# Kernel optimization log

Measured on AMD Instinct MI355X. Metric: run time of the kernel, lower is better.

Reference implementation:

```python
import jax, jax.numpy as jnp
import numpy as np


def _hippo_scale_params(N, L):
    """Replicates HiPPOScale.__init__ for discretization='bilinear' (pure numpy)."""
    q = np.arange(N, dtype=np.float64)
    col, row = np.meshgrid(q, q)
    r = 2 * q + 1
    M = -(np.where(row >= col, r, 0) - np.diag(q))
    T = np.sqrt(np.diag(2 * q + 1))
    A = T @ M @ np.linalg.inv(T)          # (N, N)
    B = np.diag(T)                         # (N,)
    ts = np.arange(1, L + 1, dtype=np.float64)[:, None, None]  # (L,1,1)
    At = A[None] / ts                      # A / t, batched over t
    I = np.eye(N, dtype=np.float64)
    Mm = I[None] - 0.5 * At
    Nn = I[None] + 0.5 * At
    A_stacked = np.linalg.solve(Mm, Nn)                      # (L, N, N)
    Bt = B[None, :] / ts[:, 0, :]                             # (L, N)
    B_stacked = np.linalg.solve(Mm, Bt[..., None])[..., 0]    # (L, N)
    return A_stacked.astype(np.float32), B_stacked.astype(np.float32)


def setup_inputs() -> dict:
    N, L, Bsz = 64, 4096, 64
    key = jax.random.key(0)
    A_st, B_st = _hippo_scale_params(N, L)
    inputs = jax.random.normal(key, (L, Bsz), dtype=jnp.float32)
    return {
        "inputs": inputs,                       # (L, B)
        "A_stacked": jnp.asarray(A_st),         # (L, N, N)
        "B_stacked": jnp.asarray(B_st),         # (L, N)
    }


def reference(inputs, A_stacked, B_stacked):
    # u[t, b, :] = inputs[t, b] * B_stacked[t, :]   -> (L, B, N)
    u = inputs[..., None] * B_stacked[:, None, :]

    # x[t] = A[t] @ x[t-1] + u[t], x[-1] = 0  (time-varying linear recurrence).
    # The torch code computes this via a divide-and-conquer unroll; here we use
    # the equivalent parallel associative scan with elements (A, u) and
    # composition (A2@A1, A2@u1 + u2).
    def combine(e1, e2):
        a1, u1 = e1
        a2, u2 = e2
        a = jnp.matmul(a2, a1)                                  # (l, N, N)
        v = jnp.einsum('...ij,...bj->...bi', a2, u1) + u2       # (l, B, N)
        return (a, v)

    _, x = jax.lax.associative_scan(combine, (A_stacked, u))
    return x  # (L, B, N)
```

## Files before the change

### kernel.cpp

```cpp
#include <hip/hip_runtime.h>

#define TL 4096
#define NB 64
#define CH 8
#define CN 512
#define AS 72

typedef __attribute__((ext_vector_type(8))) short short8;
typedef __attribute__((ext_vector_type(4))) short short4v;
typedef __attribute__((ext_vector_type(4))) float floatx4;

__device__ inline floatx4 mfma_bf16(short8 a, short8 b, floatx4 c) {
    return __builtin_amdgcn_mfma_f32_16x16x32_bf16(a, b, c, 0, 0, 0);
}

__device__ inline void split_bf16(float x, short& h, short& l) {
    union { float f; unsigned u; } v; v.f = x;
    unsigned uh = v.u + 0x7FFFu + ((v.u >> 16) & 1u);
    h = (short)(uh >> 16);
    union { unsigned u; float f; } hv; hv.u = ((unsigned)(unsigned short)h) << 16;
    float r = x - hv.f;
    union { float f; unsigned u; } rv; rv.f = r;
    unsigned ul = rv.u + 0x7FFFu + ((rv.u >> 16) & 1u);
    l = (short)(ul >> 16);
}

__global__ __launch_bounds__(256, 2)
void hippo_phase1(const float* __restrict__ inp, const float* __restrict__ Ag,
                  const float* __restrict__ Bst,
                  float* __restrict__ PT, float* __restrict__ VT)
{
    __shared__ short Ah[NB][AS], Al[NB][AS];
    __shared__ short SBh[NB][AS], SBl[NB][AS];
    __shared__ short VBh[NB][AS], VBl[NB][AS];
    __shared__ float btl[NB], itl[NB];

    const int tid  = threadIdx.x;
    const int c    = blockIdx.x;
    const int t0   = c * CH;
    const int w    = tid >> 6, lane = tid & 63;
    const int quad = lane >> 4, l15 = lane & 15;

#pragma unroll
    for (int q = 0; q < 16; ++q) {
        int f = tid + q * 256;
        int n = f >> 6, k = f & 63;
        SBh[n][k] = (n == k) ? (short)0x3F80 : (short)0;
        SBl[n][k] = 0; VBh[n][k] = 0; VBl[n][k] = 0;
    }

    float4 pre[4];
    {
        const float4* Ap = (const float4*)(Ag + (size_t)t0 * 4096);
#pragma unroll
        for (int q = 0; q < 4; ++q) pre[q] = Ap[tid + q * 256];
    }

    floatx4 accS[4], accV[4];

    for (int s = 0; s < CH; ++s) {
        int t = t0 + s;
#pragma unroll
        for (int q = 0; q < 4; ++q) {
            int f = tid + q * 256;
            int m = f >> 4, k0 = (f & 15) * 4;
            float vv[4] = {pre[q].x, pre[q].y, pre[q].z, pre[q].w};
            short4v h4, l4;
#pragma unroll
            for (int r = 0; r < 4; ++r) { short hh, ll; split_bf16(vv[r], hh, ll); h4[r]=hh; l4[r]=ll; }
            *(short4v*)&Ah[m][k0] = h4;
            *(short4v*)&Al[m][k0] = l4;
        }
        if (tid < 64) { btl[tid] = Bst[(size_t)t*64 + tid]; itl[tid] = inp[(size_t)t*64 + tid]; }
        if (s + 1 < CH) {
            const float4* Ap = (const float4*)(Ag + (size_t)(t+1) * 4096);
#pragma unroll
            for (int q = 0; q < 4; ++q) pre[q] = Ap[tid + q * 256];
        }
        __syncthreads();

#pragma unroll
        for (int ni = 0; ni < 4; ++ni) {
            float ib = itl[16*ni + l15];
#pragma unroll
            for (int r = 0; r < 4; ++r) {
                accS[ni][r] = 0.0f;
                accV[ni][r] = btl[16*w + 4*quad + r] * ib;
            }
        }
#pragma unroll
        for (int kc = 0; kc < 2; ++kc) {
            int ko = 32*kc + 8*quad;
            short8 aH = *(const short8*)&Ah[16*w + l15][ko];
            short8 aL = *(const short8*)&Al[16*w + l15][ko];
#pragma unroll
            for (int ni = 0; ni < 4; ++ni) {
                int n = 16*ni + l15;
                short8 sH = *(const short8*)&SBh[n][ko];
                short8 sL = *(const short8*)&SBl[n][ko];
                accS[ni] = mfma_bf16(aH, sH, accS[ni]);
                accS[ni] = mfma_bf16(aH, sL, accS[ni]);
                accS[ni] = mfma_bf16(aL, sH, accS[ni]);
                short8 vH = *(const short8*)&VBh[n][ko];
                short8 vL = *(const short8*)&VBl[n][ko];
                accV[ni] = mfma_bf16(aH, vH, accV[ni]);
                accV[ni] = mfma_bf16(aH, vL, accV[ni]);
                accV[ni] = mfma_bf16(aL, vH, accV[ni]);
            }
        }
        __syncthreads();

        if (s + 1 < CH) {
#pragma unroll
            for (int ni = 0; ni < 4; ++ni) {
                int cc = 16*ni + l15, r0 = 16*w + 4*quad;
                short4v h4, l4;
#pragma unroll
                for (int r = 0; r < 4; ++r) { short hh,ll; split_bf16(accS[ni][r],hh,ll); h4[r]=hh; l4[r]=ll; }
                *(short4v*)&SBh[cc][r0] = h4; *(short4v*)&SBl[cc][r0] = l4;
#pragma unroll
                for (int r = 0; r < 4; ++r) { short hh,ll; split_bf16(accV[ni][r],hh,ll); h4[r]=hh; l4[r]=ll; }
                *(short4v*)&VBh[cc][r0] = h4; *(short4v*)&VBl[cc][r0] = l4;
            }
        }
    }
#pragma unroll
    for (int ni = 0; ni < 4; ++ni) {
        int cc = 16*ni + l15, r0 = 16*w + 4*quad;
        *(floatx4*)(PT + (size_t)c*4096 + cc*64 + r0) = accS[ni];
        *(floatx4*)(VT + (size_t)c*4096 + cc*64 + r0) = accV[ni];
    }
}

__global__ __launch_bounds__(256, 2)
void hippo_seqscan(float* __restrict__ PT, float* __restrict__ VT,
                   int bstride, int off0, int estride)
{
    __shared__ short PAh[NB][AS], PAl[NB][AS];
    __shared__ short PBh[NB][AS], PBl[NB][AS];
    __shared__ short VBh[NB][AS], VBl[NB][AS];

    const int tid  = threadIdx.x;
    const int base = blockIdx.x * bstride + off0;
    const int w    = tid >> 6, lane = tid & 63;
    const int quad = lane >> 4, l15 = lane & 15;

    {
        const float* p0 = PT + (size_t)base * 4096;
        const float* v0 = VT + (size_t)base * 4096;
#pragma unroll
        for (int q = 0; q < 4; ++q) {
            int f = tid + q * 256;
            int n = f >> 4, k0 = (f & 15) * 4;
            float4 pp = *(const float4*)(p0 + n * 64 + k0);
            float4 vv = *(const float4*)(v0 + n * 64 + k0);
            float pa[4] = {pp.x, pp.y, pp.z, pp.w};
            float va[4] = {vv.x, vv.y, vv.z, vv.w};
            short4v ph4, pl4, vh4, vl4;
#pragma unroll
            for (int r = 0; r < 4; ++r) {
                short hh, ll;
                split_bf16(pa[r], hh, ll); ph4[r] = hh; pl4[r] = ll;
                split_bf16(va[r], hh, ll); vh4[r] = hh; vl4[r] = ll;
            }
            *(short4v*)&PBh[n][k0] = ph4; *(short4v*)&PBl[n][k0] = pl4;
            *(short4v*)&VBh[n][k0] = vh4; *(short4v*)&VBl[n][k0] = vl4;
        }
    }

    float4 preA[4], preV[4];
    {
        const float* pc = PT + (size_t)(base + estride) * 4096;
        const float* vc = VT + (size_t)(base + estride) * 4096;
#pragma unroll
        for (int q = 0; q < 4; ++q) {
            int f = tid + q * 256;
            int k = f & 63, m0 = (f >> 6) * 4;
            preA[q] = *(const float4*)(pc + k * 64 + m0);
        }
#pragma unroll
        for (int ni = 0; ni < 4; ++ni) {
            int cc = 16 * ni + l15, r0 = 16 * w + 4 * quad;
            preV[ni] = *(const float4*)(vc + cc * 64 + r0);
        }
    }

    for (int i = 1; i < 8; ++i) {
#pragma unroll
        for (int q = 0; q < 4; ++q) {
            int f = tid + q * 256;
            int k = f & 63, m0 = (f >> 6) * 4;
            float vv[4] = {preA[q].x, preA[q].y, preA[q].z, preA[q].w};
#pragma unroll
            for (int r = 0; r < 4; ++r) {
                short hh, ll; split_bf16(vv[r], hh, ll);
                PAh[m0 + r][k] = hh; PAl[m0 + r][k] = ll;
            }
        }
        floatx4 accP[4], accV[4];
#pragma unroll
        for (int ni = 0; ni < 4; ++ni) {
            accV[ni][0] = preV[ni].x; accV[ni][1] = preV[ni].y;
            accV[ni][2] = preV[ni].z; accV[ni][3] = preV[ni].w;
            accP[ni][0] = accP[ni][1] = accP[ni][2] = accP[ni][3] = 0.0f;
        }
        if (i + 1 < 8) {
            const float* pc = PT + (size_t)(base + (i + 1) * estride) * 4096;
            const float* vc = VT + (size_t)(base + (i + 1) * estride) * 4096;
#pragma unroll
            for (int q = 0; q < 4; ++q) {
                int f = tid + q * 256;
                int k = f & 63, m0 = (f >> 6) * 4;
                preA[q] = *(const float4*)(pc + k * 64 + m0);
            }
#pragma unroll
            for (int ni = 0; ni < 4; ++ni) {
                int cc = 16 * ni + l15, r0 = 16 * w + 4 * quad;
                preV[ni] = *(const float4*)(vc + cc * 64 + r0);
            }
        }
        __syncthreads();

#pragma unroll
        for (int kc = 0; kc < 2; ++kc) {
            int ko = 32 * kc + 8 * quad;
            short8 aH = *(const short8*)&PAh[16 * w + l15][ko];
            short8 aL = *(const short8*)&PAl[16 * w + l15][ko];
#pragma unroll
            for (int ni = 0; ni < 4; ++ni) {
                int n = 16 * ni + l15;
                short8 pH = *(const short8*)&PBh[n][ko];
                short8 pL = *(const short8*)&PBl[n][ko];
                accP[ni] = mfma_bf16(aH, pH, accP[ni]);
                accP[ni] = mfma_bf16(aH, pL, accP[ni]);
                accP[ni] = mfma_bf16(aL, pH, accP[ni]);
                short8 vH = *(const short8*)&VBh[n][ko];
                short8 vL = *(const short8*)&VBl[n][ko];
                accV[ni] = mfma_bf16(aH, vH, accV[ni]);
                accV[ni] = mfma_bf16(aH, vL, accV[ni]);
                accV[ni] = mfma_bf16(aL, vH, accV[ni]);
            }
        }
        __syncthreads();

        int idx = base + i * estride;
#pragma unroll
        for (int ni = 0; ni < 4; ++ni) {
            int cc = 16 * ni + l15, r0 = 16 * w + 4 * quad;
            *(floatx4*)(PT + (size_t)idx * 4096 + cc * 64 + r0) = accP[ni];
            *(floatx4*)(VT + (size_t)idx * 4096 + cc * 64 + r0) = accV[ni];
            short4v h4, l4;
#pragma unroll
            for (int r = 0; r < 4; ++r) { short hh,ll; split_bf16(accP[ni][r],hh,ll); h4[r]=hh; l4[r]=ll; }
            *(short4v*)&PBh[cc][r0] = h4; *(short4v*)&PBl[cc][r0] = l4;
#pragma unroll
            for (int r = 0; r < 4; ++r) { short hh,ll; split_bf16(accV[ni][r],hh,ll); h4[r]=hh; l4[r]=ll; }
            *(short4v*)&VBh[cc][r0] = h4; *(short4v*)&VBl[cc][r0] = l4;
        }
    }
}

__global__ __launch_bounds__(256, 2)
void hippo_s3(float* __restrict__ PT, const float* __restrict__ VT)
{
    __shared__ short PAh[NB][AS], PAl[NB][AS];
    __shared__ short EBh[NB][AS], EBl[NB][AS];
    const int tid = threadIdx.x;
    const int w = tid >> 6, lane = tid & 63, quad = lane >> 4, l15 = lane & 15;

#pragma unroll
    for (int q = 0; q < 16; ++q) {
        int f = tid + q * 256; EBh[f >> 6][f & 63] = 0; EBl[f >> 6][f & 63] = 0;
    }
    for (int s = 0; s < 7; ++s) {
        int idx = 64 * s + 63;
        const float* pc = PT + (size_t)idx * 4096;
        const float* vc = VT + (size_t)idx * 4096;
#pragma unroll
        for (int q = 0; q < 4; ++q) {
            int f = tid + q * 256;
            int k = f & 63, m0 = (f >> 6) * 4;
            float4 v = *(const float4*)(pc + k * 64 + m0);
            float vv[4] = {v.x, v.y, v.z, v.w};
#pragma unroll
            for (int r = 0; r < 4; ++r) {
                short hh, ll; split_bf16(vv[r], hh, ll);
                PAh[m0 + r][k] = hh; PAl[m0 + r][k] = ll;
            }
        }
        floatx4 acc[4];
#pragma unroll
        for (int ni = 0; ni < 4; ++ni) {
            int cc = 16 * ni + l15, r0 = 16 * w + 4 * quad;
            float4 vv = *(const float4*)(vc + cc * 64 + r0);
            acc[ni][0] = vv.x; acc[ni][1] = vv.y; acc[ni][2] = vv.z; acc[ni][3] = vv.w;
        }
        __syncthreads();
#pragma unroll
        for (int kc = 0; kc < 2; ++kc) {
            int ko = 32 * kc + 8 * quad;
            short8 aH = *(const short8*)&PAh[16 * w + l15][ko];
            short8 aL = *(const short8*)&PAl[16 * w + l15][ko];
#pragma unroll
            for (int ni = 0; ni < 4; ++ni) {
                int n = 16 * ni + l15;
                short8 eH = *(const short8*)&EBh[n][ko];
                short8 eL = *(const short8*)&EBl[n][ko];
                acc[ni] = mfma_bf16(aH, eH, acc[ni]);
                acc[ni] = mfma_bf16(aH, eL, acc[ni]);
                acc[ni] = mfma_bf16(aL, eH, acc[ni]);
            }
        }
        __syncthreads();
#pragma unroll
        for (int ni = 0; ni < 4; ++ni) {
            int cc = 16 * ni + l15, r0 = 16 * w + 4 * quad;
            *(floatx4*)(PT + (size_t)idx * 4096 + cc * 64 + r0) = acc[ni];
            short4v h4, l4;
#pragma unroll
            for (int r = 0; r < 4; ++r) { short hh,ll; split_bf16(acc[ni][r],hh,ll); h4[r]=hh; l4[r]=ll; }
            *(short4v*)&EBh[cc][r0] = h4; *(short4v*)&EBl[cc][r0] = l4;
        }
    }
}

__global__ __launch_bounds__(256, 2)
void hippo_phase3(const float* __restrict__ inp, const float* __restrict__ Ag,
                  const float* __restrict__ Bst, const float* __restrict__ PT,
                  const float* __restrict__ VT, float* __restrict__ out)
{
    __shared__ short Ah[NB][AS], Al[NB][AS];
    __shared__ short XBh[NB][AS], XBl[NB][AS];
    __shared__ float btl[NB], itl[NB];

    const int tid = threadIdx.x, c = blockIdx.x, t0 = c * CH;
    const int w = tid>>6, lane = tid&63, quad = lane>>4, l15 = lane&15;
    const int sup = c >> 6, g = c >> 3, gi = g & 7, j = c & 7;

    float4 pre[4];
    {
        const float4* Ap = (const float4*)(Ag + (size_t)t0 * 4096);
#pragma unroll
        for (int q = 0; q < 4; ++q) pre[q] = Ap[tid + q * 256];
    }

    if (sup == 0) {
#pragma unroll
        for (int q = 0; q < 16; ++q) { int f = tid + q*256; XBh[f>>6][f&63] = 0; XBl[f>>6][f&63] = 0; }
    } else {
        const float* e = PT + (size_t)(64*(sup-1) + 63) * 4096;
#pragma unroll
        for (int q = 0; q < 4; ++q) {
            int f = tid + q*256; int b = f>>4, k0 = (f&15)*4;
            float4 v = *(const float4*)(e + b*64 + k0);
            float va[4] = {v.x,v.y,v.z,v.w};
            short4v h4, l4;
#pragma unroll
            for (int r=0;r<4;++r){short hh,ll;split_bf16(va[r],hh,ll);h4[r]=hh;l4[r]=ll;}
            *(short4v*)&XBh[b][k0] = h4; *(short4v*)&XBl[b][k0] = l4;
        }
    }

    auto combine = [&](int idx) {
        const float* pc = PT + (size_t)idx * 4096;
        const float* vc = VT + (size_t)idx * 4096;
#pragma unroll
        for (int q = 0; q < 4; ++q) {
            int f = tid + q*256;
            int k = f & 63, m0 = (f>>6)*4;
            float4 v = *(const float4*)(pc + k*64 + m0);
            float vv[4] = {v.x,v.y,v.z,v.w};
#pragma unroll
            for (int r = 0; r < 4; ++r) { short hh,ll; split_bf16(vv[r],hh,ll); Ah[m0+r][k]=hh; Al[m0+r][k]=ll; }
        }
        floatx4 acc[4];
#pragma unroll
        for (int ni = 0; ni < 4; ++ni) {
            int cc = 16*ni + l15, r0 = 16*w + 4*quad;
            float4 vv = *(const float4*)(vc + cc*64 + r0);
            acc[ni][0]=vv.x; acc[ni][1]=vv.y; acc[ni][2]=vv.z; acc[ni][3]=vv.w;
        }
        __syncthreads();
#pragma unroll
        for (int kc = 0; kc < 2; ++kc) {
            int ko = 32*kc + 8*quad;
            short8 aH = *(const short8*)&Ah[16*w + l15][ko];
            short8 aL = *(const short8*)&Al[16*w + l15][ko];
#pragma unroll
            for (int ni = 0; ni < 4; ++ni) {
                int n = 16*ni + l15;
                short8 xH = *(const short8*)&XBh[n][ko];
                short8 xL = *(const short8*)&XBl[n][ko];
                acc[ni] = mfma_bf16(aH, xH, acc[ni]);
                acc[ni] = mfma_bf16(aH, xL, acc[ni]);
                acc[ni] = mfma_bf16(aL, xH, acc[ni]);
            }
        }
        __syncthreads();
#pragma unroll
        for (int ni = 0; ni < 4; ++ni) {
            int cc = 16*ni + l15, r0 = 16*w + 4*quad;
            short4v h4, l4;
#pragma unroll
            for (int r=0;r<4;++r){short hh,ll;split_bf16(acc[ni][r],hh,ll);h4[r]=hh;l4[r]=ll;}
            *(short4v*)&XBh[cc][r0] = h4; *(short4v*)&XBl[cc][r0] = l4;
        }
    };
    if (gi) combine(8*g - 1);
    if (j)  combine(c - 1);

    floatx4 acc[4];
    for (int s = 0; s < CH; ++s) {
        int t = t0 + s;
#pragma unroll
        for (int q = 0; q < 4; ++q) {
            int f = tid + q*256; int m = f>>4, k0 = (f&15)*4;
            float vv[4] = {pre[q].x,pre[q].y,pre[q].z,pre[q].w};
            short4v h4, l4;
#pragma unroll
            for (int r=0;r<4;++r){short hh,ll;split_bf16(vv[r],hh,ll);h4[r]=hh;l4[r]=ll;}
            *(short4v*)&Ah[m][k0] = h4; *(short4v*)&Al[m][k0] = l4;
        }
        if (tid < 64) { btl[tid] = Bst[(size_t)t*64 + tid]; itl[tid] = inp[(size_t)t*64 + tid]; }
        if (s + 1 < CH) {
            const float4* Ap = (const float4*)(Ag + (size_t)(t+1) * 4096);
#pragma unroll
            for (int q = 0; q < 4; ++q) pre[q] = Ap[tid + q * 256];
        }
        __syncthreads();

#pragma unroll
        for (int ni = 0; ni < 4; ++ni) {
            float ib = itl[16*ni + l15];
#pragma unroll
            for (int r = 0; r < 4; ++r) acc[ni][r] = btl[16*w + 4*quad + r] * ib;
        }
#pragma unroll
        for (int kc = 0; kc < 2; ++kc) {
            int ko = 32*kc + 8*quad;
            short8 aH = *(const short8*)&Ah[16*w + l15][ko];
            short8 aL = *(const short8*)&Al[16*w + l15][ko];
#pragma unroll
            for (int ni = 0; ni < 4; ++ni) {
                int n = 16*ni + l15;
                short8 xH = *(const short8*)&XBh[n][ko];
                short8 xL = *(const short8*)&XBl[n][ko];
                acc[ni] = mfma_bf16(aH, xH, acc[ni]);
                acc[ni] = mfma_bf16(aH, xL, acc[ni]);
                acc[ni] = mfma_bf16(aL, xH, acc[ni]);
            }
        }
        __syncthreads();
#pragma unroll
        for (int ni = 0; ni < 4; ++ni) {
            int cc = 16*ni + l15, r0 = 16*w + 4*quad;
            *(floatx4*)(out + (size_t)t*4096 + cc*64 + r0) = acc[ni];
            if (s + 1 < CH) {
                short4v h4, l4;
#pragma unroll
                for (int r=0;r<4;++r){short hh,ll;split_bf16(acc[ni][r],hh,ll);h4[r]=hh;l4[r]=ll;}
                *(short4v*)&XBh[cc][r0] = h4; *(short4v*)&XBl[cc][r0] = l4;
            }
        }
    }
}

extern "C" void kernel_launch(void* const* d_in, const int* in_sizes, int n_in,
                              void* d_out, int out_size, void* d_ws, size_t ws_size,
                              hipStream_t stream)
{
    const float* inp = (const float*)d_in[0];
    const float* A   = (const float*)d_in[1];
    const float* Bst = (const float*)d_in[2];
    float* out = (float*)d_out;
    float* ws  = (float*)d_ws;

    float* PT = ws;
    float* VT = ws + (size_t)CN * 4096;

    hippo_phase1<<<CN, 256, 0, stream>>>(inp, A, Bst, PT, VT);
    hippo_seqscan<<<64, 256, 0, stream>>>(PT, VT, 8, 0, 1);
    hippo_seqscan<<<8, 256, 0, stream>>>(PT, VT, 64, 7, 8);
    hippo_s3<<<1, 256, 0, stream>>>(PT, VT);
    hippo_phase3<<<CN, 256, 0, stream>>>(inp, A, Bst, PT, VT, out);
}
```

Before: 208.6 us.

## Store chunk transition matrices pre-split as packed bf16 hi/lo in row-major layout

Chunk transition matrices are now written to the workspace as packed 32-bit words holding the bf16 high and low halves, in a row-major (m,k) layout. Consumers in seqscan, s3 and phase3 can then unpack them with shifts and vectorized shared-memory stores instead of re-running the float split and doing scattered transposed LDS writes. The bf16 rounding now calls the HIP intrinsic rather than hand-written bit arithmetic. In exchange, producers do the split plus strided scalar global stores, and s3 overwrites some slots with float data that phase3 reinterprets as float, which couples the kernels through a shared buffer holding mixed formats.

```diff
diff --git a/kernel.cpp b/kernel.cpp
--- a/kernel.cpp
+++ b/kernel.cpp
@@ -1,4 +1,5 @@
 #include <hip/hip_runtime.h>
+#include <hip/hip_bf16.h>
 
 #define TL 4096
 #define NB 64
@@ -9,26 +10,28 @@
 typedef __attribute__((ext_vector_type(8))) short short8;
 typedef __attribute__((ext_vector_type(4))) short short4v;
 typedef __attribute__((ext_vector_type(4))) float floatx4;
+typedef __attribute__((ext_vector_type(4))) unsigned int uint4v;
 
 __device__ inline floatx4 mfma_bf16(short8 a, short8 b, floatx4 c) {
     return __builtin_amdgcn_mfma_f32_16x16x32_bf16(a, b, c, 0, 0, 0);
 }
 
+__device__ inline short bf16_rne(float x) {
+    union { __hip_bfloat16 b; unsigned short s; } u;
+    u.b = __float2bfloat16(x);
+    return (short)u.s;
+}
+
 __device__ inline void split_bf16(float x, short& h, short& l) {
-    union { float f; unsigned u; } v; v.f = x;
-    unsigned uh = v.u + 0x7FFFu + ((v.u >> 16) & 1u);
-    h = (short)(uh >> 16);
+    h = bf16_rne(x);
     union { unsigned u; float f; } hv; hv.u = ((unsigned)(unsigned short)h) << 16;
-    float r = x - hv.f;
-    union { float f; unsigned u; } rv; rv.f = r;
-    unsigned ul = rv.u + 0x7FFFu + ((rv.u >> 16) & 1u);
-    l = (short)(ul >> 16);
+    l = bf16_rne(x - hv.f);
 }
 
 __global__ __launch_bounds__(256, 2)
 void hippo_phase1(const float* __restrict__ inp, const float* __restrict__ Ag,
                   const float* __restrict__ Bst,
-                  float* __restrict__ PT, float* __restrict__ VT)
+                  unsigned* __restrict__ P32, float* __restrict__ VT)
 {
     __shared__ short Ah[NB][AS], Al[NB][AS];
     __shared__ short SBh[NB][AS], SBl[NB][AS];
@@ -124,16 +127,21 @@
             }
         }
     }
+    unsigned* po = P32 + (size_t)c * 4096;
 #pragma unroll
     for (int ni = 0; ni < 4; ++ni) {
         int cc = 16*ni + l15, r0 = 16*w + 4*quad;
-        *(floatx4*)(PT + (size_t)c*4096 + cc*64 + r0) = accS[ni];
         *(floatx4*)(VT + (size_t)c*4096 + cc*64 + r0) = accV[ni];
+#pragma unroll
+        for (int r = 0; r < 4; ++r) {
+            short hh, ll; split_bf16(accS[ni][r], hh, ll);
+            po[(r0 + r)*64 + cc] = ((unsigned)(unsigned short)hh << 16) | (unsigned)(unsigned short)ll;
+        }
     }
 }
 
 __global__ __launch_bounds__(256, 2)
-void hippo_seqscan(float* __restrict__ PT, float* __restrict__ VT,
+void hippo_seqscan(unsigned* __restrict__ P32, float* __restrict__ VT,
                    int bstride, int off0, int estride)
 {
     __shared__ short PAh[NB][AS], PAl[NB][AS];
@@ -146,37 +154,41 @@
     const int quad = lane >> 4, l15 = lane & 15;
 
     {
-        const float* p0 = PT + (size_t)base * 4096;
-        const float* v0 = VT + (size_t)base * 4096;
+        const unsigned* p0 = P32 + (size_t)base * 4096;
+        const float*    v0 = VT  + (size_t)base * 4096;
+#pragma unroll
+        for (int q = 0; q < 4; ++q) {
+            int f = tid + q * 256;
+            int k = f & 63, m0 = (f >> 6) * 4;
+            uint4v pk = *(const uint4v*)(p0 + k * 64 + m0);
+#pragma unroll
+            for (int r = 0; r < 4; ++r) {
+                PBh[m0 + r][k] = (short)(pk[r] >> 16);
+                PBl[m0 + r][k] = (short)(pk[r] & 0xFFFFu);
+            }
+        }
 #pragma unroll
         for (int q = 0; q < 4; ++q) {
             int f = tid + q * 256;
             int n = f >> 4, k0 = (f & 15) * 4;
-            float4 pp = *(const float4*)(p0 + n * 64 + k0);
             float4 vv = *(const float4*)(v0 + n * 64 + k0);
-            float pa[4] = {pp.x, pp.y, pp.z, pp.w};
             float va[4] = {vv.x, vv.y, vv.z, vv.w};
-            short4v ph4, pl4, vh4, vl4;
-#pragma unroll
-            for (int r = 0; r < 4; ++r) {
-                short hh, ll;
-                split_bf16(pa[r], hh, ll); ph4[r] = hh; pl4[r] = ll;
-                split_bf16(va[r], hh, ll); vh4[r] = hh; vl4[r] = ll;
-            }
-            *(short4v*)&PBh[n][k0] = ph4; *(short4v*)&PBl[n][k0] = pl4;
+            short4v vh4, vl4;
+#pragma unroll
+            for (int r = 0; r < 4; ++r) { short hh, ll; split_bf16(va[r], hh, ll); vh4[r]=hh; vl4[r]=ll; }
             *(short4v*)&VBh[n][k0] = vh4; *(short4v*)&VBl[n][k0] = vl4;
         }
     }
 
-    float4 preA[4], preV[4];
+    uint4v preA[4]; float4 preV[4];
     {
-        const float* pc = PT + (size_t)(base + estride) * 4096;
-        const float* vc = VT + (size_t)(base + estride) * 4096;
+        const unsigned* pc = P32 + (size_t)(base + estride) * 4096;
+        const float*    vc = VT  + (size_t)(base + estride) * 4096;
 #pragma unroll
         for (int q = 0; q < 4; ++q) {
             int f = tid + q * 256;
-            int k = f & 63, m0 = (f >> 6) * 4;
-            preA[q] = *(const float4*)(pc + k * 64 + m0);
+            int m = f >> 4, k0 = (f & 15) * 4;
+            preA[q] = *(const uint4v*)(pc + m * 64 + k0);
         }
 #pragma unroll
         for (int ni = 0; ni < 4; ++ni) {
@@ -189,13 +201,12 @@
 #pragma unroll
         for (int q = 0; q < 4; ++q) {
             int f = tid + q * 256;
-            int k = f & 63, m0 = (f >> 6) * 4;
-            float vv[4] = {preA[q].x, preA[q].y, preA[q].z, preA[q].w};
-#pragma unroll
-            for (int r = 0; r < 4; ++r) {
-                short hh, ll; split_bf16(vv[r], hh, ll);
-                PAh[m0 + r][k] = hh; PAl[m0 + r][k] = ll;
-            }
+            int m = f >> 4, k0 = (f & 15) * 4;
+            short4v h4, l4;
+#pragma unroll
+            for (int r = 0; r < 4; ++r) { h4[r] = (short)(preA[q][r] >> 16); l4[r] = (short)(preA[q][r] & 0xFFFFu); }
+            *(short4v*)&PAh[m][k0] = h4;
+            *(short4v*)&PAl[m][k0] = l4;
         }
         floatx4 accP[4], accV[4];
 #pragma unroll
@@ -205,13 +216,13 @@
             accP[ni][0] = accP[ni][1] = accP[ni][2] = accP[ni][3] = 0.0f;
         }
         if (i + 1 < 8) {
-            const float* pc = PT + (size_t)(base + (i + 1) * estride) * 4096;
-            const float* vc = VT + (size_t)(base + (i + 1) * estride) * 4096;
+            const unsigned* pc = P32 + (size_t)(base + (i + 1) * estride) * 4096;
+            const float*    vc = VT  + (size_t)(base + (i + 1) * estride) * 4096;
 #pragma unroll
             for (int q = 0; q < 4; ++q) {
                 int f = tid + q * 256;
-                int k = f & 63, m0 = (f >> 6) * 4;
-                preA[q] = *(const float4*)(pc + k * 64 + m0);
+                int m = f >> 4, k0 = (f & 15) * 4;
+                preA[q] = *(const uint4v*)(pc + m * 64 + k0);
             }
 #pragma unroll
             for (int ni = 0; ni < 4; ++ni) {
@@ -244,14 +255,18 @@
         __syncthreads();
 
         int idx = base + i * estride;
+        unsigned* po = P32 + (size_t)idx * 4096;
 #pragma unroll
         for (int ni = 0; ni < 4; ++ni) {
             int cc = 16 * ni + l15, r0 = 16 * w + 4 * quad;
-            *(floatx4*)(PT + (size_t)idx * 4096 + cc * 64 + r0) = accP[ni];
             *(floatx4*)(VT + (size_t)idx * 4096 + cc * 64 + r0) = accV[ni];
             short4v h4, l4;
 #pragma unroll
-            for (int r = 0; r < 4; ++r) { short hh,ll; split_bf16(accP[ni][r],hh,ll); h4[r]=hh; l4[r]=ll; }
+            for (int r = 0; r < 4; ++r) {
+                short hh, ll; split_bf16(accP[ni][r], hh, ll);
+                po[(r0 + r) * 64 + cc] = ((unsigned)(unsigned short)hh << 16) | (unsigned)(unsigned short)ll;
+                h4[r] = hh; l4[r] = ll;
+            }
             *(short4v*)&PBh[cc][r0] = h4; *(short4v*)&PBl[cc][r0] = l4;
 #pragma unroll
             for (int r = 0; r < 4; ++r) { short hh,ll; split_bf16(accV[ni][r],hh,ll); h4[r]=hh; l4[r]=ll; }
@@ -261,7 +276,7 @@
 }
 
 __global__ __launch_bounds__(256, 2)
-void hippo_s3(float* __restrict__ PT, const float* __restrict__ VT)
+void hippo_s3(unsigned* __restrict__ P32, const float* __restrict__ VT)
 {
     __shared__ short PAh[NB][AS], PAl[NB][AS];
     __shared__ short EBh[NB][AS], EBl[NB][AS];
@@ -274,19 +289,18 @@
     }
     for (int s = 0; s < 7; ++s) {
         int idx = 64 * s + 63;
-        const float* pc = PT + (size_t)idx * 4096;
-        const float* vc = VT + (size_t)idx * 4096;
+        const unsigned* pc = P32 + (size_t)idx * 4096;
+        const float*    vc = VT  + (size_t)idx * 4096;
 #pragma unroll
         for (int q = 0; q < 4; ++q) {
             int f = tid + q * 256;
-            int k = f & 63, m0 = (f >> 6) * 4;
-            float4 v = *(const float4*)(pc + k * 64 + m0);
-            float vv[4] = {v.x, v.y, v.z, v.w};
-#pragma unroll
-            for (int r = 0; r < 4; ++r) {
-                short hh, ll; split_bf16(vv[r], hh, ll);
-                PAh[m0 + r][k] = hh; PAl[m0 + r][k] = ll;
-            }
+            int m = f >> 4, k0 = (f & 15) * 4;
+            uint4v pk = *(const uint4v*)(pc + m * 64 + k0);
+            short4v h4, l4;
+#pragma unroll
+            for (int r = 0; r < 4; ++r) { h4[r] = (short)(pk[r] >> 16); l4[r] = (short)(pk[r] & 0xFFFFu); }
+            *(short4v*)&PAh[m][k0] = h4;
+            *(short4v*)&PAl[m][k0] = l4;
         }
         floatx4 acc[4];
 #pragma unroll
@@ -312,10 +326,11 @@
             }
         }
         __syncthreads();
+        float* eo = (float*)(P32 + (size_t)idx * 4096);
 #pragma unroll
         for (int ni = 0; ni < 4; ++ni) {
             int cc = 16 * ni + l15, r0 = 16 * w + 4 * quad;
-            *(floatx4*)(PT + (size_t)idx * 4096 + cc * 64 + r0) = acc[ni];
+            *(floatx4*)(eo + cc * 64 + r0) = acc[ni];
             short4v h4, l4;
 #pragma unroll
             for (int r = 0; r < 4; ++r) { short hh,ll; split_bf16(acc[ni][r],hh,ll); h4[r]=hh; l4[r]=ll; }
@@ -326,7 +341,7 @@
 
 __global__ __launch_bounds__(256, 2)
 void hippo_phase3(const float* __restrict__ inp, const float* __restrict__ Ag,
-                  const float* __restrict__ Bst, const float* __restrict__ PT,
+                  const float* __restrict__ Bst, const unsigned* __restrict__ P32,
                   const float* __restrict__ VT, float* __restrict__ out)
 {
     __shared__ short Ah[NB][AS], Al[NB][AS];
@@ -348,7 +363,7 @@
 #pragma unroll
         for (int q = 0; q < 16; ++q) { int f = tid + q*256; XBh[f>>6][f&63] = 0; XBl[f>>6][f&63] = 0; }
     } else {
-        const float* e = PT + (size_t)(64*(sup-1) + 63) * 4096;
+        const float* e = (const float*)(P32 + (size_t)(64*(sup-1) + 63) * 4096);
 #pragma unroll
         for (int q = 0; q < 4; ++q) {
             int f = tid + q*256; int b = f>>4, k0 = (f&15)*4;
@@ -362,16 +377,18 @@
     }
 
     auto combine = [&](int idx) {
-        const float* pc = PT + (size_t)idx * 4096;
-        const float* vc = VT + (size_t)idx * 4096;
+        const unsigned* pc = P32 + (size_t)idx * 4096;
+        const float*    vc = VT  + (size_t)idx * 4096;
 #pragma unroll
         for (int q = 0; q < 4; ++q) {
             int f = tid + q*256;
-            int k = f & 63, m0 = (f>>6)*4;
-            float4 v = *(const float4*)(pc + k*64 + m0);
-            float vv[4] = {v.x,v.y,v.z,v.w};
-#pragma unroll
-            for (int r = 0; r < 4; ++r) { short hh,ll; split_bf16(vv[r],hh,ll); Ah[m0+r][k]=hh; Al[m0+r][k]=ll; }
+            int m = f >> 4, k0 = (f & 15) * 4;
+            uint4v pk = *(const uint4v*)(pc + m * 64 + k0);
+            short4v h4, l4;
+#pragma unroll
+            for (int r = 0; r < 4; ++r) { h4[r] = (short)(pk[r] >> 16); l4[r] = (short)(pk[r] & 0xFFFFu); }
+            *(short4v*)&Ah[m][k0] = h4;
+            *(short4v*)&Al[m][k0] = l4;
         }
         floatx4 acc[4];
 #pragma unroll
@@ -475,12 +492,12 @@
     float* out = (float*)d_out;
     float* ws  = (float*)d_ws;
 
-    float* PT = ws;
-    float* VT = ws + (size_t)CN * 4096;
-
-    hippo_phase1<<<CN, 256, 0, stream>>>(inp, A, Bst, PT, VT);
-    hippo_seqscan<<<64, 256, 0, stream>>>(PT, VT, 8, 0, 1);
-    hippo_seqscan<<<8, 256, 0, stream>>>(PT, VT, 64, 7, 8);
-    hippo_s3<<<1, 256, 0, stream>>>(PT, VT);
-    hippo_phase3<<<CN, 256, 0, stream>>>(inp, A, Bst, PT, VT, out);
-}
+    unsigned* P32 = (unsigned*)ws;
+    float*    VT  = ws + (size_t)CN * 4096;
+
+    hippo_phase1<<<CN, 256, 0, stream>>>(inp, A, Bst, P32, VT);
+    hippo_seqscan<<<64, 256, 0, stream>>>(P32, VT, 8, 0, 1);
+    hippo_seqscan<<<8, 256, 0, stream>>>(P32, VT, 64, 7, 8);
+    hippo_s3<<<1, 256, 0, stream>>>(P32, VT);
+    hippo_phase3<<<CN, 256, 0, stream>>>(inp, A, Bst, P32, VT, out);
+}
```

After: 184.0 us. -11.8%, faster.
